# Kernel tuning notes

Measured on AMD Instinct MI355X. Metric: run time of the kernel, lower is better.

The kernel has to match this reference:

```python
import jax, jax.numpy as jnp
import numpy as np

B, C, H, W = 8, 64, 128, 128
O, KS, STRIDE, PAD = 64, 3, 1, 1
K = KS * KS


def setup_inputs() -> dict:
    key = jax.random.key(0)
    k1, k2, k3 = jax.random.split(key, 3)
    x = jax.random.normal(k1, (B, C, H, W), dtype=jnp.float32)
    offset = jax.random.normal(k2, (B, 2 * K, H, W), dtype=jnp.float32)
    weight = jax.random.normal(k3, (O, C, KS, KS), dtype=jnp.float32)
    bias = jnp.zeros((O,), dtype=jnp.float32)
    return {"x": x, "offset": offset, "weight": weight, "bias": bias}


def _deform_conv(x, offset, weight, bias, ks=KS, stride=STRIDE, pad=PAD):
    Bx, Cx, Hx, Wx = x.shape
    Kk = ks * ks
    Ho = (Hx + 2 * pad - ks) // stride + 1
    Wo = (Wx + 2 * pad - ks) // stride + 1
    x_pad = jnp.pad(x, ((0, 0), (0, 0), (pad, pad), (pad, pad)))
    Hp, Wp = Hx + 2 * pad, Wx + 2 * pad
    # base grid (top-left tap, padded coords) -- matches torch code exactly
    ys = jnp.arange(Ho, dtype=x.dtype) * stride
    xs = jnp.arange(Wo, dtype=x.dtype) * stride
    off = offset.reshape(Bx, Kk, 2, Ho, Wo).astype(x.dtype)
    gx = off[:, :, 0] + xs[None, None, None, :]   # [B,K,Ho,Wo]
    gy = off[:, :, 1] + ys[None, None, :, None]
    # bilinear sample with zeros padding (grid_sample align_corners=True round-trips
    # normalization exactly, so we sample at (gy,gx) directly)
    x0 = jnp.floor(gx); y0 = jnp.floor(gy)
    wx1 = gx - x0; wx0 = 1.0 - wx1
    wy1 = gy - y0; wy0 = 1.0 - wy1
    x_flat = x_pad.reshape(Bx, Cx, Hp * Wp)

    def gather(yi, xi, w):
        valid = (xi >= 0) & (xi <= Wp - 1) & (yi >= 0) & (yi <= Hp - 1)
        xi_c = jnp.clip(xi, 0, Wp - 1).astype(jnp.int32)
        yi_c = jnp.clip(yi, 0, Hp - 1).astype(jnp.int32)
        idx = (yi_c * Wp + xi_c).reshape(Bx, -1)           # [B, K*Ho*Wo]
        g = jnp.take_along_axis(x_flat, idx[:, None, :], axis=2)  # [B,C,K*Ho*Wo]
        wv = (w * valid.astype(x.dtype)).reshape(Bx, 1, -1)
        return g * wv

    acc = (gather(y0, x0, wy0 * wx0)
           + gather(y0, x0 + 1.0, wy0 * wx1)
           + gather(y0 + 1.0, x0, wy1 * wx0)
           + gather(y0 + 1.0, x0 + 1.0, wy1 * wx1))
    # channel layout after torch.cat over k: index = k*C + c (k-major)
    sampled = acc.reshape(Bx, Cx, Kk, Ho, Wo).transpose(0, 2, 1, 3, 4)
    sampled = sampled.reshape(Bx, Kk * Cx, Ho, Wo)
    # torch flattens weight as (c, kh, kw) -> index = c*K + k; faithful mismatch
    w_flat = weight.reshape(weight.shape[0], -1).astype(sampled.dtype)  # [O, C*K]
    out = jnp.einsum('oi,bihw->bohw', w_flat, sampled)
    return out + bias[None, :, None, None]


def reference(x, offset, weight, bias):
    return _deform_conv(x, offset, weight, bias)
```

## Files before the change

kernel.cpp:

```cpp
#include <hip/hip_runtime.h>
#include <hip/hip_bf16.h>

#define BB 8
#define CC 64
#define OO 64
#define HH 128
#define WWI 128
#define HWSZ (HH * WWI)
#define KK 9
#define II (KK * CC)

#define PXW 16
#define PYH 16
#define WNX 24
#define WNY 24
#define WROWS (WNX * WNY)

typedef __attribute__((ext_vector_type(8))) _Float16 half8;
typedef __attribute__((ext_vector_type(2))) _Float16 h2;
typedef __attribute__((ext_vector_type(4))) float f32x4;
typedef __attribute__((ext_vector_type(4))) unsigned int uint4v;

__device__ __forceinline__ int iclamp(int v, int lo, int hi) {
    return v < lo ? lo : (v > hi ? hi : v);
}
__device__ __forceinline__ unsigned short f2h(float f) {
    union { _Float16 h; unsigned short s; } v;
    v.h = (_Float16)f;
    return v.s;
}
__device__ __forceinline__ h2 u2h(unsigned u) {
    union { unsigned u; h2 h; } v;
    v.u = u;
    return v.h;
}

__global__ __launch_bounds__(256) void prep_xt(const float* __restrict__ x,
                                               unsigned short* __restrict__ xt) {
    __shared__ float tile[64][65];
    const int blk = blockIdx.x;
    const int b = blk & 7;
    const int p0 = (blk >> 3) * 64;
    const int t = threadIdx.x;
    const int a = t >> 6;
    const int q = t & 63;
    const float* xb = x + (size_t)b * CC * HWSZ + p0;
#pragma unroll
    for (int r = 0; r < 16; ++r) {
        int c = r * 4 + a;
        tile[c][q] = xb[(size_t)c * HWSZ + q];
    }
    __syncthreads();
    unsigned short* xo = xt + ((size_t)b * HWSZ + p0) * CC;
#pragma unroll
    for (int r = 0; r < 16; ++r) {
        int pl = r * 4 + a;
        xo[(size_t)pl * CC + q] = f2h(tile[q][pl]);
    }
}

__global__ void prep_waf(const float* __restrict__ w, unsigned short* __restrict__ waf) {
    int tid = blockIdx.x * 256 + threadIdx.x;
    if (tid < 72 * 512) {
        int slab = tid >> 9;
        int r = tid & 511;
        int l = r >> 3, j = r & 7;
        int m = slab & 3;
        int kc = (slab >> 2) & 1;
        int k = slab >> 3;
        int o = m * 16 + (l & 15);
        int i = k * 64 + kc * 32 + (l >> 4) * 8 + j;
        waf[tid] = f2h(w[(size_t)o * II + i]);
    }
}

__global__ __launch_bounds__(512, 2) void deform_mfma9(
        const unsigned short* __restrict__ xt,
        const float* __restrict__ off,
        const unsigned short* __restrict__ waf,
        const float* __restrict__ bias,
        float* __restrict__ out) {
    extern __shared__ unsigned short win[];

    const int blk = blockIdx.x;
    const int b = blk & 7;
    const int pidx = blk >> 3;
    const int y0 = (pidx >> 3) * PYH;
    const int x0 = (pidx & 7) * PXW;
    const int xleft = x0 - 4, ytop = y0 - 4;

    const int t = threadIdx.x;
    const int wave = t >> 6;
    const int lane = t & 63;
    const int fm = lane & 15;
    const int hi = lane >> 4;
    const int c0s = hi * 8;
    const int c1s = 32 + hi * 8;

    const unsigned short* xtb = xt + (size_t)b * HWSZ * CC;
    const float* offpx = off + (size_t)b * 2 * KK * HWSZ
                             + (size_t)(y0 + wave * 2) * WWI + x0 + fm;

    float ox[3][2], oy[3][2];
#pragma unroll
    for (int k = 0; k < 2; ++k) {
#pragma unroll
        for (int nt = 0; nt < 2; ++nt) {
            ox[k][nt] = offpx[(size_t)(2 * k + 0) * HWSZ + nt * WWI];
            oy[k][nt] = offpx[(size_t)(2 * k + 1) * HWSZ + nt * WWI];
        }
    }

    {
        const int tch = t & 7;
        const int rb = t >> 3;
#pragma unroll
        for (int sw = 0; sw < 9; ++sw) {
            const int r = sw * 64 + rb;
            const int wy = r / WNX, wx = r - wy * WNX;
            const int cy = ytop + wy, cx = xleft + wx;
            if (((unsigned)cy < (unsigned)HH) && ((unsigned)cx < (unsigned)WWI)) {
                const uint4v v = *(const uint4v*)(xtb + (size_t)(cy * WWI + cx) * CC + tch * 8);
                *(uint4v*)&win[r * CC + ((tch ^ (r & 7)) << 3)] = v;
            }
        }
    }
    __syncthreads();

    f32x4 acc[2][4];
#pragma unroll
    for (int nt = 0; nt < 2; ++nt)
#pragma unroll
        for (int m = 0; m < 4; ++m) acc[nt][m] = (f32x4)(0.0f);

    uint4v cb[2][8];
    float  cw[2][4];
    bool   inwf[2];
    int    gidx[2][4];
    half8  afb[2][8];

#define LDSRD(r, kc) (*(const uint4v*)&win[(r) * CC + ((((hi) + ((kc) << 2)) ^ ((r) & 7)) << 3)])

#define ISSUE(u) do {                                                           \
        if ((((u) & 1) == 0) && (((u) >> 1) + 2 < KK)) {                        \
            _Pragma("unroll")                                                   \
            for (int nt = 0; nt < 2; ++nt) {                                    \
                ox[(((u) >> 1) + 2) % 3][nt] =                                  \
                    offpx[(size_t)(2 * (((u) >> 1) + 2) + 0) * HWSZ + nt * WWI];\
                oy[(((u) >> 1) + 2) % 3][nt] =                                  \
                    offpx[(size_t)(2 * (((u) >> 1) + 2) + 1) * HWSZ + nt * WWI];\
            }                                                                   \
        }                                                                       \
        if (((u) & 1) == 0) {                                                   \
            const unsigned short* wk = waf + (size_t)((u) >> 1) * 8 * 512 + lane * 8; \
            _Pragma("unroll")                                                   \
            for (int q = 0; q < 8; ++q)                                         \
                afb[((u) >> 1) & 1][q] = *(const half8*)(wk + (size_t)q * 512); \
        }                                                                       \
        const float gx = ox[((u) >> 1) % 3][(u) & 1] + (float)(x0 + fm);        \
        const float gy = oy[((u) >> 1) % 3][(u) & 1] + (float)(y0 + wave * 2 + ((u) & 1)); \
        const float fxf = floorf(gx), fyf = floorf(gy);                         \
        const float fx = gx - fxf, fy = gy - fyf;                               \
        const int ux0 = (int)fxf - 1, ux1 = (int)fxf;                           \
        const int uy0 = (int)fyf - 1, uy1 = (int)fyf;                           \
        const float vx0 = ((unsigned)ux0 < (unsigned)WWI) ? 1.0f : 0.0f;        \
        const float vx1 = ((unsigned)ux1 < (unsigned)WWI) ? 1.0f : 0.0f;        \
        const float vy0 = ((unsigned)uy0 < (unsigned)HH) ? 1.0f : 0.0f;         \
        const float vy1 = ((unsigned)uy1 < (unsigned)HH) ? 1.0f : 0.0f;         \
        cw[(u) & 1][0] = (1.0f - fy) * (1.0f - fx) * vy0 * vx0;                 \
        cw[(u) & 1][1] = (1.0f - fy) * fx          * vy0 * vx1;                 \
        cw[(u) & 1][2] = fy          * (1.0f - fx) * vy1 * vx0;                 \
        cw[(u) & 1][3] = fy          * fx          * vy1 * vx1;                 \
        const int cx0 = iclamp(ux0, 0, WWI - 1), cx1 = iclamp(ux1, 0, WWI - 1); \
        const int cy0 = iclamp(uy0, 0, HH - 1),  cy1 = iclamp(uy1, 0, HH - 1);  \
        inwf[(u) & 1] = (cx0 >= xleft) & (cx1 <= xleft + WNX - 1)               \
                      & (cy0 >= ytop) & (cy1 <= ytop + WNY - 1);                \
        gidx[(u) & 1][0] = cy0 * WWI + cx0;  gidx[(u) & 1][1] = cy0 * WWI + cx1;\
        gidx[(u) & 1][2] = cy1 * WWI + cx0;  gidx[(u) & 1][3] = cy1 * WWI + cx1;\
        const int wx0 = iclamp(cx0 - xleft, 0, WNX - 1);                        \
        const int wx1 = iclamp(cx1 - xleft, 0, WNX - 1);                        \
        const int wy0 = iclamp(cy0 - ytop, 0, WNY - 1);                         \
        const int wy1 = iclamp(cy1 - ytop, 0, WNY - 1);                         \
        const int r00 = wy0 * WNX + wx0, r01 = wy0 * WNX + wx1;                 \
        const int r10 = wy1 * WNX + wx0, r11 = wy1 * WNX + wx1;                 \
        cb[(u) & 1][0] = LDSRD(r00, 0);  cb[(u) & 1][1] = LDSRD(r00, 1);        \
        cb[(u) & 1][2] = LDSRD(r01, 0);  cb[(u) & 1][3] = LDSRD(r01, 1);        \
        cb[(u) & 1][4] = LDSRD(r10, 0);  cb[(u) & 1][5] = LDSRD(r10, 1);        \
        cb[(u) & 1][6] = LDSRD(r11, 0);  cb[(u) & 1][7] = LDSRD(r11, 1);        \
    } while (0)

#define PROC(u) do {                                                            \
        asm volatile("" : "+v"(cb[(u) & 1][0]), "+v"(cb[(u) & 1][1]),           \
                          "+v"(cb[(u) & 1][2]), "+v"(cb[(u) & 1][3]),           \
                          "+v"(cb[(u) & 1][4]), "+v"(cb[(u) & 1][5]),           \
                          "+v"(cb[(u) & 1][6]), "+v"(cb[(u) & 1][7]));          \
        uint4v A0 = cb[(u) & 1][0], A1 = cb[(u) & 1][1];                        \
        uint4v B0 = cb[(u) & 1][2], B1 = cb[(u) & 1][3];                        \
        uint4v C0 = cb[(u) & 1][4], C1 = cb[(u) & 1][5];                        \
        uint4v D0 = cb[(u) & 1][6], D1 = cb[(u) & 1][7];                        \
        if (!inwf[(u) & 1]) {                                                   \
            const unsigned short* g00 = xtb + (size_t)gidx[(u) & 1][0] * CC;    \
            const unsigned short* g01 = xtb + (size_t)gidx[(u) & 1][1] * CC;    \
            const unsigned short* g10 = xtb + (size_t)gidx[(u) & 1][2] * CC;    \
            const unsigned short* g11 = xtb + (size_t)gidx[(u) & 1][3] * CC;    \
            A0 = *(const uint4v*)(g00 + c0s);  A1 = *(const uint4v*)(g00 + c1s);\
            B0 = *(const uint4v*)(g01 + c0s);  B1 = *(const uint4v*)(g01 + c1s);\
            C0 = *(const uint4v*)(g10 + c0s);  C1 = *(const uint4v*)(g10 + c1s);\
            D0 = *(const uint4v*)(g11 + c0s);  D1 = *(const uint4v*)(g11 + c1s);\
        }                                                                       \
        const _Float16 hw00 = (_Float16)cw[(u) & 1][0];                         \
        const _Float16 hw01 = (_Float16)cw[(u) & 1][1];                         \
        const _Float16 hw10 = (_Float16)cw[(u) & 1][2];                         \
        const _Float16 hw11 = (_Float16)cw[(u) & 1][3];                         \
        const h2 w00v = {hw00, hw00}, w01v = {hw01, hw01};                      \
        const h2 w10v = {hw10, hw10}, w11v = {hw11, hw11};                      \
        half8 bf0, bf1;                                                         \
        h2* rp0 = (h2*)&bf0;                                                    \
        h2* rp1 = (h2*)&bf1;                                                    \
        _Pragma("unroll")                                                       \
        for (int i = 0; i < 4; ++i) {                                           \
            h2 r0 = u2h(A0[i]) * w00v;                                          \
            r0 += u2h(B0[i]) * w01v;                                            \
            r0 += u2h(C0[i]) * w10v;                                            \
            r0 += u2h(D0[i]) * w11v;                                            \
            rp0[i] = r0;                                                        \
            h2 r1 = u2h(A1[i]) * w00v;                                          \
            r1 += u2h(B1[i]) * w01v;                                            \
            r1 += u2h(C1[i]) * w10v;                                            \
            r1 += u2h(D1[i]) * w11v;                                            \
            rp1[i] = r1;                                                        \
        }                                                                       \
        _Pragma("unroll")                                                       \
        for (int m = 0; m < 4; ++m)                                             \
            acc[(u) & 1][m] = __builtin_amdgcn_mfma_f32_16x16x32_f16(           \
                afb[((u) >> 1) & 1][m], bf0, acc[(u) & 1][m], 0, 0, 0);         \
        _Pragma("unroll")                                                       \
        for (int m = 0; m < 4; ++m)                                             \
            acc[(u) & 1][m] = __builtin_amdgcn_mfma_f32_16x16x32_f16(           \
                afb[((u) >> 1) & 1][4 + m], bf1, acc[(u) & 1][m], 0, 0, 0);     \
    } while (0)

    ISSUE(0);  ISSUE(1);
    PROC(0);   ISSUE(2);
    PROC(1);   ISSUE(3);
    PROC(2);   ISSUE(4);
    PROC(3);   ISSUE(5);
    PROC(4);   ISSUE(6);
    PROC(5);   ISSUE(7);
    PROC(6);   ISSUE(8);
    PROC(7);   ISSUE(9);
    PROC(8);   ISSUE(10);
    PROC(9);   ISSUE(11);
    PROC(10);  ISSUE(12);
    PROC(11);  ISSUE(13);
    PROC(12);  ISSUE(14);
    PROC(13);  ISSUE(15);
    PROC(14);  ISSUE(16);
    PROC(15);  ISSUE(17);
    PROC(16);
    PROC(17);

#undef ISSUE
#undef PROC
#undef LDSRD

#pragma unroll
    for (int nt = 0; nt < 2; ++nt) {
        float* outb = out + (size_t)b * OO * HWSZ
                          + (size_t)(y0 + wave * 2 + nt) * WWI + x0 + fm;
#pragma unroll
        for (int m = 0; m < 4; ++m) {
            const int ob = m * 16 + hi * 4;
            const float4 bs = *(const float4*)(bias + ob);
#pragma unroll
            for (int j = 0; j < 4; ++j) {
                outb[(size_t)(ob + j) * HWSZ] = acc[nt][m][j] + ((const float*)&bs)[j];
            }
        }
    }
}

__global__ __launch_bounds__(256) void deform_conv_fallback(
        const float* __restrict__ x, const float* __restrict__ off,
        const float* __restrict__ wmat, const float* __restrict__ bias,
        float* __restrict__ out) {
    const int b = blockIdx.y;
    const int p = blockIdx.x * 256 + threadIdx.x;
    const int wo = p & (WWI - 1);
    const int ho = p >> 7;
    const float* xb = x + (size_t)b * CC * HWSZ;
    const float* offb = off + (size_t)b * 2 * KK * HWSZ + p;
    float acc[OO];
#pragma unroll
    for (int o = 0; o < OO; ++o) acc[o] = 0.0f;
#pragma unroll 1
    for (int k = 0; k < KK; ++k) {
        const float gx = offb[(size_t)(2 * k + 0) * HWSZ] + (float)wo;
        const float gy = offb[(size_t)(2 * k + 1) * HWSZ] + (float)ho;
        const float fxf = floorf(gx), fyf = floorf(gy);
        const float fx = gx - fxf, fy = gy - fyf;
        const int ux0 = (int)fxf - 1, ux1 = (int)fxf;
        const int uy0 = (int)fyf - 1, uy1 = (int)fyf;
        const float vx0 = ((unsigned)ux0 < (unsigned)WWI) ? 1.0f : 0.0f;
        const float vx1 = ((unsigned)ux1 < (unsigned)WWI) ? 1.0f : 0.0f;
        const float vy0 = ((unsigned)uy0 < (unsigned)HH) ? 1.0f : 0.0f;
        const float vy1 = ((unsigned)uy1 < (unsigned)HH) ? 1.0f : 0.0f;
        const float w00 = (1.0f - fy) * (1.0f - fx) * vy0 * vx0;
        const float w01 = (1.0f - fy) * fx * vy0 * vx1;
        const float w10 = fy * (1.0f - fx) * vy1 * vx0;
        const float w11 = fy * fx * vy1 * vx1;
        const int cx0 = iclamp(ux0, 0, WWI - 1), cx1 = iclamp(ux1, 0, WWI - 1);
        const int cy0 = iclamp(uy0, 0, HH - 1), cy1 = iclamp(uy1, 0, HH - 1);
        const int i00 = cy0 * WWI + cx0, i01 = cy0 * WWI + cx1;
        const int i10 = cy1 * WWI + cx0, i11 = cy1 * WWI + cx1;
#pragma unroll 4
        for (int c = 0; c < CC; ++c) {
            const float* xc = xb + (size_t)c * HWSZ;
            const float v = w00 * xc[i00] + w01 * xc[i01] + w10 * xc[i10] + w11 * xc[i11];
            const float* wrow = wmat + (size_t)(k * CC + c);
#pragma unroll
            for (int o = 0; o < OO; ++o) acc[o] = fmaf(wrow[(size_t)o * II], v, acc[o]);
        }
    }
    float* outb = out + (size_t)b * OO * HWSZ + p;
#pragma unroll
    for (int o = 0; o < OO; ++o) outb[(size_t)o * HWSZ] = acc[o] + bias[o];
}

extern "C" void kernel_launch(void* const* d_in, const int* in_sizes, int n_in,
                              void* d_out, int out_size, void* d_ws, size_t ws_size,
                              hipStream_t stream) {
    const float* x    = (const float*)d_in[0];
    const float* off  = (const float*)d_in[1];
    const float* w    = (const float*)d_in[2];
    const float* bias = (const float*)d_in[3];
    float* out = (float*)d_out;

    const size_t xt_bytes  = (size_t)BB * HWSZ * CC * sizeof(unsigned short);
    const size_t waf_bytes = (size_t)72 * 512 * sizeof(unsigned short);

    if (ws_size >= xt_bytes + waf_bytes) {
        unsigned short* xt  = (unsigned short*)d_ws;
        unsigned short* wfp = (unsigned short*)((char*)d_ws + xt_bytes);
        prep_xt<<<dim3((HWSZ / 64) * BB), 256, 0, stream>>>(x, xt);
        prep_waf<<<(72 * 512 + 255) / 256, 256, 0, stream>>>(w, wfp);
        deform_mfma9<<<dim3(BB * (HH / PYH) * (WWI / PXW)), dim3(512),
                       WROWS * CC * sizeof(unsigned short), stream>>>(
            xt, off, wfp, bias, out);
    } else {
        deform_conv_fallback<<<dim3(HWSZ / 256, BB), 256, 0, stream>>>(x, off, w, bias, out);
    }
}
```

Before: 46.54 us.

## Merge prep kernels, strengthen LDS swizzle, raise wave priority around MFMA

```diff
diff --git a/kernel.cpp b/kernel.cpp
--- a/kernel.cpp
+++ b/kernel.cpp
@@ -1,5 +1,4 @@
 #include <hip/hip_runtime.h>
-#include <hip/hip_bf16.h>
 
 #define BB 8
 #define CC 64
@@ -16,6 +15,8 @@
 #define WNY 24
 #define WROWS (WNX * WNY)
 
+#define MIXR(r) (((r) ^ ((r) >> 3)) & 7)
+
 typedef __attribute__((ext_vector_type(8))) _Float16 half8;
 typedef __attribute__((ext_vector_type(2))) _Float16 h2;
 typedef __attribute__((ext_vector_type(4))) float f32x4;
@@ -35,46 +36,48 @@
     return v.h;
 }
 
-__global__ __launch_bounds__(256) void prep_xt(const float* __restrict__ x,
-                                               unsigned short* __restrict__ xt) {
-    __shared__ float tile[64][65];
+__global__ __launch_bounds__(256) void prep_all(const float* __restrict__ x,
+                                                unsigned short* __restrict__ xt,
+                                                const float* __restrict__ w,
+                                                unsigned short* __restrict__ waf) {
     const int blk = blockIdx.x;
-    const int b = blk & 7;
-    const int p0 = (blk >> 3) * 64;
     const int t = threadIdx.x;
-    const int a = t >> 6;
-    const int q = t & 63;
-    const float* xb = x + (size_t)b * CC * HWSZ + p0;
-#pragma unroll
-    for (int r = 0; r < 16; ++r) {
-        int c = r * 4 + a;
-        tile[c][q] = xb[(size_t)c * HWSZ + q];
-    }
-    __syncthreads();
-    unsigned short* xo = xt + ((size_t)b * HWSZ + p0) * CC;
-#pragma unroll
-    for (int r = 0; r < 16; ++r) {
-        int pl = r * 4 + a;
-        xo[(size_t)pl * CC + q] = f2h(tile[q][pl]);
-    }
-}
-
-__global__ void prep_waf(const float* __restrict__ w, unsigned short* __restrict__ waf) {
-    int tid = blockIdx.x * 256 + threadIdx.x;
-    if (tid < 72 * 512) {
-        int slab = tid >> 9;
-        int r = tid & 511;
-        int l = r >> 3, j = r & 7;
-        int m = slab & 3;
-        int kc = (slab >> 2) & 1;
-        int k = slab >> 3;
-        int o = m * 16 + (l & 15);
-        int i = k * 64 + kc * 32 + (l >> 4) * 8 + j;
-        waf[tid] = f2h(w[(size_t)o * II + i]);
-    }
-}
-
-__global__ __launch_bounds__(512, 2) void deform_mfma9(
+    if (blk < 2048) {
+        __shared__ float tile[64][65];
+        const int b = blk & 7;
+        const int p0 = (blk >> 3) * 64;
+        const int a = t >> 6;
+        const int q = t & 63;
+        const float* xb = x + (size_t)b * CC * HWSZ + p0;
+#pragma unroll
+        for (int r = 0; r < 16; ++r) {
+            int c = r * 4 + a;
+            tile[c][q] = xb[(size_t)c * HWSZ + q];
+        }
+        __syncthreads();
+        unsigned short* xo = xt + ((size_t)b * HWSZ + p0) * CC;
+#pragma unroll
+        for (int r = 0; r < 16; ++r) {
+            int pl = r * 4 + a;
+            xo[(size_t)pl * CC + q] = f2h(tile[q][pl]);
+        }
+    } else {
+        int tid = (blk - 2048) * 256 + t;
+        if (tid < 72 * 512) {
+            int slab = tid >> 9;
+            int r = tid & 511;
+            int l = r >> 3, j = r & 7;
+            int m = slab & 3;
+            int kc = (slab >> 2) & 1;
+            int k = slab >> 3;
+            int o = m * 16 + (l & 15);
+            int i = k * 64 + kc * 32 + (l >> 4) * 8 + j;
+            waf[tid] = f2h(w[(size_t)o * II + i]);
+        }
+    }
+}
+
+__global__ __launch_bounds__(512, 2) void deform_mfma13(
         const unsigned short* __restrict__ xt,
         const float* __restrict__ off,
         const unsigned short* __restrict__ waf,
@@ -121,7 +124,7 @@
             const int cy = ytop + wy, cx = xleft + wx;
             if (((unsigned)cy < (unsigned)HH) && ((unsigned)cx < (unsigned)WWI)) {
                 const uint4v v = *(const uint4v*)(xtb + (size_t)(cy * WWI + cx) * CC + tch * 8);
-                *(uint4v*)&win[r * CC + ((tch ^ (r & 7)) << 3)] = v;
+                *(uint4v*)&win[r * CC + ((tch ^ MIXR(r)) << 3)] = v;
             }
         }
     }
@@ -139,7 +142,7 @@
     int    gidx[2][4];
     half8  afb[2][8];
 
-#define LDSRD(r, kc) (*(const uint4v*)&win[(r) * CC + ((((hi) + ((kc) << 2)) ^ ((r) & 7)) << 3)])
+#define LDSRD(r, kc) (*(const uint4v*)&win[(r) * CC + ((((hi) + ((kc) << 2)) ^ MIXR(r)) << 3)])
 
 #define ISSUE(u) do {                                                           \
         if ((((u) & 1) == 0) && (((u) >> 1) + 2 < KK)) {                        \
@@ -230,6 +233,7 @@
             r1 += u2h(D1[i]) * w11v;                                            \
             rp1[i] = r1;                                                        \
         }                                                                       \
+        __builtin_amdgcn_s_setprio(1);                                          \
         _Pragma("unroll")                                                       \
         for (int m = 0; m < 4; ++m)                                             \
             acc[(u) & 1][m] = __builtin_amdgcn_mfma_f32_16x16x32_f16(           \
@@ -238,6 +242,7 @@
         for (int m = 0; m < 4; ++m)                                             \
             acc[(u) & 1][m] = __builtin_amdgcn_mfma_f32_16x16x32_f16(           \
                 afb[((u) >> 1) & 1][4 + m], bf1, acc[(u) & 1][m], 0, 0, 0);     \
+        __builtin_amdgcn_s_setprio(0);                                          \
     } while (0)
 
     ISSUE(0);  ISSUE(1);
@@ -340,13 +345,12 @@
     const size_t waf_bytes = (size_t)72 * 512 * sizeof(unsigned short);
 
     if (ws_size >= xt_bytes + waf_bytes) {
-        unsigned short* xt  = (unsigned short*)d_ws;
+        unsigned short* xtp = (unsigned short*)d_ws;
         unsigned short* wfp = (unsigned short*)((char*)d_ws + xt_bytes);
-        prep_xt<<<dim3((HWSZ / 64) * BB), 256, 0, stream>>>(x, xt);
-        prep_waf<<<(72 * 512 + 255) / 256, 256, 0, stream>>>(w, wfp);
-        deform_mfma9<<<dim3(BB * (HH / PYH) * (WWI / PXW)), dim3(512),
-                       WROWS * CC * sizeof(unsigned short), stream>>>(
-            xt, off, wfp, bias, out);
+        prep_all<<<dim3(2048 + 144), 256, 0, stream>>>(x, xtp, w, wfp);
+        deform_mfma13<<<dim3(BB * (HH / PYH) * (WWI / PXW)), dim3(512),
+                        WROWS * CC * sizeof(unsigned short), stream>>>(
+            xtp, off, wfp, bias, out);
     } else {
         deform_conv_fallback<<<dim3(HWSZ / 256, BB), 256, 0, stream>>>(x, off, w, bias, out);
     }
```

Measured after the change: 46.57 us. About the same (+0.1%).
